# Kernel tuning notes

Hardware: AMD Instinct MI355X
Metric: run time of the kernel (lower is better)

Reference implementation:

```python
import jax, jax.numpy as jnp
import numpy as np

EPS = 1e-10
N = 8192


def _plus(x):
    # relu with small positive shift, exactly as in the source
    return x * (x > EPS) + EPS * (x < EPS)


def _cbrt(x):
    return jnp.sign(x) * jnp.abs(x) ** (1.0 / 3.0)


def _quartic(a, b, c, d, e):
    # positive root of quartic, vectorized over events
    p = (8 * a * c - 3 * b ** 2) / (8 * a ** 2)
    q = (b ** 3 - 4 * a * b * c + 8 * a ** 2 * d) / (8 * a ** 3)
    d0 = c ** 2 - 3 * b * d + 12 * a * e
    d1 = 2 * c ** 3 - 9 * b * c * d + 27 * b ** 2 * e + 27 * a * d ** 2 - 72 * a * c * e
    temp1 = d1 ** 2 - 4 * d0 ** 3
    Q = _cbrt((_plus(temp1) ** 0.5 + d1) / 2)
    temp2 = -2.0 / 3.0 * p + (Q + d0 / Q) / (3 * a)
    S = _plus(temp2) ** 0.5 / 2
    temp3 = -4 * S ** 2 - 2 * p + q / S
    x1 = -b / (4 * a) - S + _plus(temp3) ** 0.5 / 2
    return x1 * (S > 0.001) * (x1 > 0.0)


def setup_inputs() -> dict:
    key = jax.random.key(0)
    t_end = 8192
    his_t = jnp.sort(jax.random.uniform(key, (N,), dtype=jnp.float32) * t_end)
    return {
        "his_t": his_t,
        "log_mu": jnp.array(np.log(1.0), dtype=jnp.float32),
        "log_zeta": jnp.array(np.log(1.0), dtype=jnp.float32),
        "c0": jnp.array(0.5, dtype=jnp.float32),
        "c1": jnp.array(0.1, dtype=jnp.float32),
        "c2": jnp.array(0.05, dtype=jnp.float32),
        "t_start": 0,
        "t_end": t_end,
    }


def reference(his_t, log_mu, log_zeta, c0, c1, c2, t_start, t_end):
    mu = jnp.exp(log_mu)
    zeta = jnp.exp(log_zeta)

    # strictly-lower-triangular pairwise time differences, clamped at 50
    dt = jnp.tril(his_t[:, None] - his_t[None, :], -1)  # [N, N]
    dt = jnp.minimum(dt, 50.0)

    # term 1: -sum log intensity at each event
    lamb = jnp.sum(jnp.tril((c2 * dt ** 2 + c1 * dt + c0) * jnp.exp(-zeta * dt), -1), -1)
    lamb = _plus(mu + lamb)
    term_1 = -jnp.sum(jnp.log(lamb))

    term_2 = mu * (t_end - t_start)

    # quartic coefficients (note: tril with k=0 here, includes the diagonal, as in the source)
    tril_exp = jnp.tril(jnp.exp(-zeta * dt))
    a_ = jnp.sum(c2 * tril_exp, -1)
    b_ = jnp.sum((c1 + 2 * c2 * dt) * tril_exp, -1)
    c_ = jnp.sum((c0 + c1 * dt + c2 * dt ** 2) * tril_exp, -1)
    a = a_ / 2.0
    b = -a_ + b_ / 2.0
    c = a_ - b_ + c_ / 2.0
    d = b_ - c_
    e = c_ + mu
    roots = _quartic(a, b, c, d, e)  # [N]

    term_2 = term_2 - jnp.sum(roots) * mu

    roots = roots + his_t
    roots = jnp.concatenate([jnp.zeros(1, dtype=his_t.dtype), roots])  # [N+1]
    neg_start = jnp.concatenate([his_t, jnp.ones(1, dtype=his_t.dtype) * t_end])  # [N+1]

    int_start = jax.nn.relu(neg_start[:, None] - his_t[None, :])  # [N+1, N]
    int_end = jax.nn.relu(roots[:, None] - his_t[None, :])  # [N+1, N]

    def antideriv(x):
        zx = zeta * x
        return jnp.exp(-zx) * (-c2 * (zx * (zx + 2) + 2) - zeta * (c1 * zx + c1 + c0 * zeta))

    term_3 = jnp.sum(antideriv(int_start) - antideriv(int_end)) / zeta ** 3
    return term_1 + term_2 + term_3
```

## Files before the change

kernel.cpp:

```cpp
#include <hip/hip_runtime.h>
#include <math.h>

#define EPSV 1e-10

__device__ __forceinline__ double dplus(double x) {
    return x > EPSV ? x : (x < EPSV ? EPSV : 0.0);
}

__device__ __forceinline__ int lower_bound_f(const float* __restrict__ arr, int n, float v) {
    int lo = 0, hi = n;
    while (lo < hi) {
        int mid = (lo + hi) >> 1;
        if (arr[mid] < v) lo = mid + 1; else hi = mid;
    }
    return lo;
}

extern "C" __global__ void __launch_bounds__(64)
row_quartic_kernel(const float* __restrict__ t, int n,
                   const float* __restrict__ log_mu_p,
                   const float* __restrict__ log_zeta_p,
                   const float* __restrict__ c0_p, const float* __restrict__ c1_p,
                   const float* __restrict__ c2_p,
                   float* __restrict__ roots_shifted,
                   double* __restrict__ p_neglog, double* __restrict__ p_root)
{
    const int i = blockIdx.x;
    const float zeta = expf(log_zeta_p[0]);
    const float c0 = c0_p[0], c1 = c1_p[0], c2 = c2_p[0];
    const float ti = t[i];

    float W = 50.0f;
    if (expf(-50.0f * zeta) * (fabsf(c0) + 50.0f * fabsf(c1) + 2500.0f * fabsf(c2) + 1.0f) > 1e-13f)
        W = 3.0e38f;
    const int jlo = lower_bound_f(t, i + 1, ti - W);

    double sa = 0.0, sb = 0.0, sc = 0.0;
    for (int j = jlo + (int)threadIdx.x; j <= i; j += 64) {
        float dt = fminf(ti - t[j], 50.0f);
        float ex = expf(-zeta * dt);
        sa += (double)(c2 * ex);
        sb += (double)((c1 + 2.0f * c2 * dt) * ex);
        sc += (double)((c0 + dt * (c1 + dt * c2)) * ex);
    }
    for (int off = 32; off > 0; off >>= 1) {
        sa += __shfl_down(sa, off);
        sb += __shfl_down(sb, off);
        sc += __shfl_down(sc, off);
    }

    if (threadIdx.x == 0) {
        const double a_ = (double)(float)sa;
        const double b_ = (double)(float)sb;
        const double c_ = (double)(float)sc;
        const double mu = exp((double)log_mu_p[0]);

        const double a = 0.5 * a_;
        const double b = -a_ + 0.5 * b_;
        const double c = a_ - b_ + 0.5 * c_;
        const double d = b_ - c_;
        const double e = c_ + mu;

        const double p  = (8.0 * a * c - 3.0 * b * b) / (8.0 * a * a);
        const double q  = (b * b * b - 4.0 * a * b * c + 8.0 * a * a * d) / (8.0 * a * a * a);
        const double d0 = c * c - 3.0 * b * d + 12.0 * a * e;
        const double d1 = 2.0 * c * c * c - 9.0 * b * c * d + 27.0 * b * b * e
                        + 27.0 * a * d * d - 72.0 * a * c * e;
        const double temp1 = d1 * d1 - 4.0 * d0 * d0 * d0;
        const double Q  = cbrt((sqrt(dplus(temp1)) + d1) * 0.5);
        const double temp2 = -(2.0 / 3.0) * p + (Q + d0 / Q) / (3.0 * a);
        const double S  = sqrt(dplus(temp2)) * 0.5;
        const double temp3 = -4.0 * S * S - 2.0 * p + q / S;
        const double x1 = -b / (4.0 * a) - S + sqrt(dplus(temp3)) * 0.5;
        const double root = (S > 0.001 && x1 > 0.0) ? x1 : 0.0;

        const double lamb = dplus(mu + (c_ - (double)c0_p[0]));
        p_neglog[i] = -log(lamb);
        p_root[i] = root;
        roots_shifted[i] = (float)root + ti;
    }
}

extern "C" __global__ void __launch_bounds__(64)
term3_kernel(const float* __restrict__ t, int n,
             const float* __restrict__ log_zeta_p,
             const float* __restrict__ c0_p, const float* __restrict__ c1_p,
             const float* __restrict__ c2_p,
             const float* __restrict__ roots_shifted,
             const int* __restrict__ t_end_p,
             double* __restrict__ p3)
{
    const int i = blockIdx.x;
    const float zeta = expf(log_zeta_p[0]);
    const float c0 = c0_p[0], c1 = c1_p[0], c2 = c2_p[0];
    const float s = (i < n) ? t[i] : (float)t_end_p[0];
    const float e = (i == 0) ? 0.0f : roots_shifted[i - 1];

    const float hi_v = fmaxf(s, e);
    const float lo_v = fminf(s, e) - 70.0f / zeta;
    const int jlo = lower_bound_f(t, n, lo_v);
    const int jhi = lower_bound_f(t, n, hi_v);

    double acc = 0.0;
    for (int j = jlo + (int)threadIdx.x; j < jhi; j += 64) {
        const float tj = t[j];
        const float xs = fmaxf(s - tj, 0.0f);
        const float xe = fmaxf(e - tj, 0.0f);
        const float zxs = zeta * xs;
        const float vs = expf(-zxs) *
            (-c2 * (zxs * (zxs + 2.0f) + 2.0f) - zeta * (c1 * zxs + c1 + c0 * zeta));
        const float zxe = zeta * xe;
        const float ve = expf(-zxe) *
            (-c2 * (zxe * (zxe + 2.0f) + 2.0f) - zeta * (c1 * zxe + c1 + c0 * zeta));
        acc += (double)(vs - ve);
    }
    for (int off = 32; off > 0; off >>= 1) acc += __shfl_down(acc, off);
    if (threadIdx.x == 0) p3[i] = acc;
}

extern "C" __global__ void __launch_bounds__(256)
reduce_kernel(int n,
              const double* __restrict__ p_neglog,
              const double* __restrict__ p_root,
              const double* __restrict__ p3,
              const float* __restrict__ log_mu_p,
              const float* __restrict__ log_zeta_p,
              const int* __restrict__ t_start_p,
              const int* __restrict__ t_end_p,
              float* __restrict__ out)
{
    double s1 = 0.0, s2 = 0.0, s3 = 0.0;
    for (int i = (int)threadIdx.x; i < n; i += 256) {
        s1 += p_neglog[i];
        s2 += p_root[i];
    }
    for (int i = (int)threadIdx.x; i < n + 1; i += 256) s3 += p3[i];

    for (int off = 32; off > 0; off >>= 1) {
        s1 += __shfl_down(s1, off);
        s2 += __shfl_down(s2, off);
        s3 += __shfl_down(s3, off);
    }
    __shared__ double l1[4], l2[4], l3[4];
    const int wave = (int)threadIdx.x >> 6;
    if ((threadIdx.x & 63) == 0) { l1[wave] = s1; l2[wave] = s2; l3[wave] = s3; }
    __syncthreads();
    if (threadIdx.x == 0) {
        const double term1 = l1[0] + l1[1] + l1[2] + l1[3];
        const double sroot = l2[0] + l2[1] + l2[2] + l2[3];
        const double raw3  = l3[0] + l3[1] + l3[2] + l3[3];
        const double mu = exp((double)log_mu_p[0]);
        const double zeta = exp((double)log_zeta_p[0]);
        const double term2 = mu * (double)(t_end_p[0] - t_start_p[0]) - sroot * mu;
        const double term3 = raw3 / (zeta * zeta * zeta);
        out[0] = (float)(term1 + term2 + term3);
    }
}

extern "C" void kernel_launch(void* const* d_in, const int* in_sizes, int n_in,
                              void* d_out, int out_size, void* d_ws, size_t ws_size,
                              hipStream_t stream)
{
    (void)n_in; (void)out_size; (void)ws_size;
    const float* his_t    = (const float*)d_in[0];
    const float* log_mu   = (const float*)d_in[1];
    const float* log_zeta = (const float*)d_in[2];
    const float* c0       = (const float*)d_in[3];
    const float* c1       = (const float*)d_in[4];
    const float* c2       = (const float*)d_in[5];
    const int*   t_start  = (const int*)d_in[6];
    const int*   t_end    = (const int*)d_in[7];
    const int n = in_sizes[0];

    double* p_neglog = (double*)d_ws;
    double* p_root   = p_neglog + n;
    double* p3       = p_root + n;
    float*  roots_shifted = (float*)(p3 + (n + 1));

    row_quartic_kernel<<<n, 64, 0, stream>>>(his_t, n, log_mu, log_zeta, c0, c1, c2,
                                             roots_shifted, p_neglog, p_root);
    term3_kernel<<<n + 1, 64, 0, stream>>>(his_t, n, log_zeta, c0, c1, c2,
                                           roots_shifted, t_end, p3);
    reduce_kernel<<<1, 256, 0, stream>>>(n, p_neglog, p_root, p3,
                                         log_mu, log_zeta, t_start, t_end,
                                         (float*)d_out);
}
```

Baseline: 103.8 us.

## Map one thread per row instead of one block per row, with block-level partial sums

The row and term-3 kernels now give each event its own thread, looping serially over the short time window, instead of giving each event a 64-thread block. The per-row quartic solve in fp64 now runs across all lanes rather than on lane 0 of many blocks. Each kernel reduces its results to one partial per 128-thread block, so the final kernel sums far fewer values. This removes the launch and scheduling cost of thousands of tiny blocks and the serialized lane-0 work. In exchange, only a few dozen blocks are launched, which leaves much of the GPU idle, and per-thread loop lengths can differ within a wave.

```diff
diff --git a/kernel.cpp b/kernel.cpp
--- a/kernel.cpp
+++ b/kernel.cpp
@@ -16,40 +16,36 @@
     return lo;
 }
 
-extern "C" __global__ void __launch_bounds__(64)
+extern "C" __global__ void __launch_bounds__(128)
 row_quartic_kernel(const float* __restrict__ t, int n,
                    const float* __restrict__ log_mu_p,
                    const float* __restrict__ log_zeta_p,
                    const float* __restrict__ c0_p, const float* __restrict__ c1_p,
                    const float* __restrict__ c2_p,
                    float* __restrict__ roots_shifted,
-                   double* __restrict__ p_neglog, double* __restrict__ p_root)
+                   double* __restrict__ pk_neglog, double* __restrict__ pk_root)
 {
-    const int i = blockIdx.x;
+    const int i = blockIdx.x * 128 + (int)threadIdx.x;
     const float zeta = expf(log_zeta_p[0]);
     const float c0 = c0_p[0], c1 = c1_p[0], c2 = c2_p[0];
-    const float ti = t[i];
 
-    float W = 50.0f;
-    if (expf(-50.0f * zeta) * (fabsf(c0) + 50.0f * fabsf(c1) + 2500.0f * fabsf(c2) + 1.0f) > 1e-13f)
-        W = 3.0e38f;
-    const int jlo = lower_bound_f(t, i + 1, ti - W);
+    double neglog = 0.0, root = 0.0;
+    if (i < n) {
+        const float ti = t[i];
+        float W = 50.0f;
+        if (expf(-50.0f * zeta) * (fabsf(c0) + 50.0f * fabsf(c1) + 2500.0f * fabsf(c2) + 1.0f) > 1e-13f)
+            W = 3.0e38f;
+        const int jlo = lower_bound_f(t, i + 1, ti - W);
 
-    double sa = 0.0, sb = 0.0, sc = 0.0;
-    for (int j = jlo + (int)threadIdx.x; j <= i; j += 64) {
-        float dt = fminf(ti - t[j], 50.0f);
-        float ex = expf(-zeta * dt);
-        sa += (double)(c2 * ex);
-        sb += (double)((c1 + 2.0f * c2 * dt) * ex);
-        sc += (double)((c0 + dt * (c1 + dt * c2)) * ex);
-    }
-    for (int off = 32; off > 0; off >>= 1) {
-        sa += __shfl_down(sa, off);
-        sb += __shfl_down(sb, off);
-        sc += __shfl_down(sc, off);
-    }
+        double sa = 0.0, sb = 0.0, sc = 0.0;
+        for (int j = jlo; j <= i; ++j) {
+            const float dt = fminf(ti - t[j], 50.0f);
+            const float ex = expf(-zeta * dt);
+            sa += (double)(c2 * ex);
+            sb += (double)((c1 + 2.0f * c2 * dt) * ex);
+            sc += (double)((c0 + dt * (c1 + dt * c2)) * ex);
+        }
 
-    if (threadIdx.x == 0) {
         const double a_ = (double)(float)sa;
         const double b_ = (double)(float)sb;
         const double c_ = (double)(float)sc;
@@ -72,87 +68,99 @@
         const double S  = sqrt(dplus(temp2)) * 0.5;
         const double temp3 = -4.0 * S * S - 2.0 * p + q / S;
         const double x1 = -b / (4.0 * a) - S + sqrt(dplus(temp3)) * 0.5;
-        const double root = (S > 0.001 && x1 > 0.0) ? x1 : 0.0;
+        root = (S > 0.001 && x1 > 0.0) ? x1 : 0.0;
 
-        const double lamb = dplus(mu + (c_ - (double)c0_p[0]));
-        p_neglog[i] = -log(lamb);
-        p_root[i] = root;
+        neglog = -log(dplus(mu + (c_ - (double)c0_p[0])));
         roots_shifted[i] = (float)root + ti;
+    }
+
+    for (int off = 32; off > 0; off >>= 1) {
+        neglog += __shfl_down(neglog, off);
+        root   += __shfl_down(root, off);
+    }
+    __shared__ double l1[2], l2[2];
+    const int wave = (int)threadIdx.x >> 6;
+    if ((threadIdx.x & 63) == 0) { l1[wave] = neglog; l2[wave] = root; }
+    __syncthreads();
+    if (threadIdx.x == 0) {
+        pk_neglog[blockIdx.x] = l1[0] + l1[1];
+        pk_root[blockIdx.x]   = l2[0] + l2[1];
     }
 }
 
-extern "C" __global__ void __launch_bounds__(64)
+extern "C" __global__ void __launch_bounds__(128)
 term3_kernel(const float* __restrict__ t, int n,
              const float* __restrict__ log_zeta_p,
              const float* __restrict__ c0_p, const float* __restrict__ c1_p,
              const float* __restrict__ c2_p,
              const float* __restrict__ roots_shifted,
              const int* __restrict__ t_end_p,
-             double* __restrict__ p3)
+             double* __restrict__ pk3)
 {
-    const int i = blockIdx.x;
+    const int i = blockIdx.x * 128 + (int)threadIdx.x;
     const float zeta = expf(log_zeta_p[0]);
     const float c0 = c0_p[0], c1 = c1_p[0], c2 = c2_p[0];
-    const float s = (i < n) ? t[i] : (float)t_end_p[0];
-    const float e = (i == 0) ? 0.0f : roots_shifted[i - 1];
-
-    const float hi_v = fmaxf(s, e);
-    const float lo_v = fminf(s, e) - 70.0f / zeta;
-    const int jlo = lower_bound_f(t, n, lo_v);
-    const int jhi = lower_bound_f(t, n, hi_v);
 
     double acc = 0.0;
-    for (int j = jlo + (int)threadIdx.x; j < jhi; j += 64) {
-        const float tj = t[j];
-        const float xs = fmaxf(s - tj, 0.0f);
-        const float xe = fmaxf(e - tj, 0.0f);
-        const float zxs = zeta * xs;
-        const float vs = expf(-zxs) *
-            (-c2 * (zxs * (zxs + 2.0f) + 2.0f) - zeta * (c1 * zxs + c1 + c0 * zeta));
-        const float zxe = zeta * xe;
-        const float ve = expf(-zxe) *
-            (-c2 * (zxe * (zxe + 2.0f) + 2.0f) - zeta * (c1 * zxe + c1 + c0 * zeta));
-        acc += (double)(vs - ve);
+    if (i <= n) {
+        const float s = (i < n) ? t[i] : (float)t_end_p[0];
+        const float e = (i == 0) ? 0.0f : roots_shifted[i - 1];
+
+        const float hi_v = fmaxf(s, e);
+        const float lo_v = fminf(s, e) - 70.0f / zeta;
+        const int jlo = lower_bound_f(t, n, lo_v);
+        const int jhi = lower_bound_f(t, n, hi_v);
+
+        for (int j = jlo; j < jhi; ++j) {
+            const float tj = t[j];
+            const float xs = fmaxf(s - tj, 0.0f);
+            const float xe = fmaxf(e - tj, 0.0f);
+            const float zxs = zeta * xs;
+            const float vs = expf(-zxs) *
+                (-c2 * (zxs * (zxs + 2.0f) + 2.0f) - zeta * (c1 * zxs + c1 + c0 * zeta));
+            const float zxe = zeta * xe;
+            const float ve = expf(-zxe) *
+                (-c2 * (zxe * (zxe + 2.0f) + 2.0f) - zeta * (c1 * zxe + c1 + c0 * zeta));
+            acc += (double)(vs - ve);
+        }
     }
+
     for (int off = 32; off > 0; off >>= 1) acc += __shfl_down(acc, off);
-    if (threadIdx.x == 0) p3[i] = acc;
+    __shared__ double l3[2];
+    const int wave = (int)threadIdx.x >> 6;
+    if ((threadIdx.x & 63) == 0) l3[wave] = acc;
+    __syncthreads();
+    if (threadIdx.x == 0) pk3[blockIdx.x] = l3[0] + l3[1];
 }
 
-extern "C" __global__ void __launch_bounds__(256)
-reduce_kernel(int n,
-              const double* __restrict__ p_neglog,
-              const double* __restrict__ p_root,
-              const double* __restrict__ p3,
-              const float* __restrict__ log_mu_p,
-              const float* __restrict__ log_zeta_p,
-              const int* __restrict__ t_start_p,
-              const int* __restrict__ t_end_p,
-              float* __restrict__ out)
+extern "C" __global__ void __launch_bounds__(64)
+finalize_kernel(int nb1, int nb2,
+                const double* __restrict__ pk_neglog,
+                const double* __restrict__ pk_root,
+                const double* __restrict__ pk3,
+                const float* __restrict__ log_mu_p,
+                const float* __restrict__ log_zeta_p,
+                const int* __restrict__ t_start_p,
+                const int* __restrict__ t_end_p,
+                float* __restrict__ out)
 {
     double s1 = 0.0, s2 = 0.0, s3 = 0.0;
-    for (int i = (int)threadIdx.x; i < n; i += 256) {
-        s1 += p_neglog[i];
-        s2 += p_root[i];
+    for (int i = (int)threadIdx.x; i < nb1; i += 64) {
+        s1 += pk_neglog[i];
+        s2 += pk_root[i];
     }
-    for (int i = (int)threadIdx.x; i < n + 1; i += 256) s3 += p3[i];
-
+    for (int i = (int)threadIdx.x; i < nb2; i += 64) s3 += pk3[i];
     for (int off = 32; off > 0; off >>= 1) {
         s1 += __shfl_down(s1, off);
         s2 += __shfl_down(s2, off);
         s3 += __shfl_down(s3, off);
     }
-    __shared__ double l1[4], l2[4], l3[4];
-    const int wave = (int)threadIdx.x >> 6;
-    if ((threadIdx.x & 63) == 0) { l1[wave] = s1; l2[wave] = s2; l3[wave] = s3; }
-    __syncthreads();
     if (threadIdx.x == 0) {
-        const double term1 = l1[0] + l1[1] + l1[2] + l1[3];
-        const double sroot = l2[0] + l2[1] + l2[2] + l2[3];
-        const double raw3  = l3[0] + l3[1] + l3[2] + l3[3];
         const double mu = exp((double)log_mu_p[0]);
         const double zeta = exp((double)log_zeta_p[0]);
-        const double term2 = mu * (double)(t_end_p[0] - t_start_p[0]) - sroot * mu;
-        const double term3 = raw3 / (zeta * zeta * zeta);
+        const double term1 = s1;
+        const double term2 = mu * (double)(t_end_p[0] - t_start_p[0]) - s2 * mu;
+        const double term3 = s3 / (zeta * zeta * zeta);
         out[0] = (float)(term1 + term2 + term3);
     }
 }
@@ -172,16 +180,19 @@
     const int*   t_end    = (const int*)d_in[7];
     const int n = in_sizes[0];
 
-    double* p_neglog = (double*)d_ws;
-    double* p_root   = p_neglog + n;
-    double* p3       = p_root + n;
-    float*  roots_shifted = (float*)(p3 + (n + 1));
+    const int nb1 = (n + 127) / 128;
+    const int nb2 = (n + 1 + 127) / 128;
 
-    row_quartic_kernel<<<n, 64, 0, stream>>>(his_t, n, log_mu, log_zeta, c0, c1, c2,
-                                             roots_shifted, p_neglog, p_root);
-    term3_kernel<<<n + 1, 64, 0, stream>>>(his_t, n, log_zeta, c0, c1, c2,
-                                           roots_shifted, t_end, p3);
-    reduce_kernel<<<1, 256, 0, stream>>>(n, p_neglog, p_root, p3,
-                                         log_mu, log_zeta, t_start, t_end,
-                                         (float*)d_out);
+    double* pk_neglog = (double*)d_ws;
+    double* pk_root   = pk_neglog + nb1;
+    double* pk3       = pk_root + nb1;
+    float*  roots_shifted = (float*)(pk3 + nb2);
+
+    row_quartic_kernel<<<nb1, 128, 0, stream>>>(his_t, n, log_mu, log_zeta, c0, c1, c2,
+                                                roots_shifted, pk_neglog, pk_root);
+    term3_kernel<<<nb2, 128, 0, stream>>>(his_t, n, log_zeta, c0, c1, c2,
+                                          roots_shifted, t_end, pk3);
+    finalize_kernel<<<1, 64, 0, stream>>>(nb1, nb2, pk_neglog, pk_root, pk3,
+                                          log_mu, log_zeta, t_start, t_end,
+                                          (float*)d_out);
 }
```

Result: faster. 100.6 us (-3.1%).
